# Optimization experiments

Hardware: AMD Instinct MI355X
Metric: run time of the kernel (lower is better)

Reference implementation:

```python
import jax, jax.numpy as jnp
import numpy as np

T, B, N = 1000, 64, 512
DT = 0.01
EL, VR, TR, TINF = -0.07, -0.07, -0.06, -0.05
A_VAL = 2.6239240169525146
A1_VAL = -0.015625353902578354
A2_VAL = -1.0590057373046875
B_VAL = 12.77495288848877
G_VAL = 45.24007797241211
K1, K2 = 200.0, 20.0
R1, R2 = 0.3858567178249359, -1.1421641111373901
C = 1.0


def setup_inputs() -> dict:
    key = jax.random.key(0)
    x = jax.random.normal(key, (T, B, N), dtype=jnp.float32)
    linear = jnp.ones((1, N), jnp.float32)
    a = jnp.full((1, N), A_VAL, jnp.float32)
    A1 = jnp.full((1, N), A1_VAL * C, jnp.float32)
    A2 = jnp.full((1, N), A2_VAL * C, jnp.float32)
    return {"x": x, "linear": linear, "a": a, "A1": A1, "A2": A2}


def _spike(v):
    # Heaviside step (forward of SurrGradSpike)
    return (v > 0).astype(v.dtype)


def reference(x, linear, a, A1, A2):
    G = G_VAL * C

    def step(state, xt):
        V, i1, i2, Thr = state
        i1 = i1 - K1 * i1 * DT
        i2 = i2 - K2 * i2 * DT
        V = V + DT * (linear * xt + i1 + i2 - G * (V - EL)) / C
        Thr = Thr + DT * (a * (V - EL) - B_VAL * (Thr - TINF))
        spk = _spike(V - Thr)
        i1 = (1.0 - spk) * i1 + spk * (R1 * i1 + A1)
        i2 = (1.0 - spk) * i2 + spk * (R2 * i2 + A2)
        Thr = (1.0 - spk) * Thr + spk * jnp.maximum(Thr, TR)
        V = (1.0 - spk) * V + spk * VR
        return (V, i1, i2, Thr), spk

    Bd, Nd = x.shape[1], x.shape[2]
    init = (
        jnp.full((Bd, Nd), EL, x.dtype),   # V
        jnp.zeros((Bd, Nd), x.dtype),      # i1
        jnp.zeros((Bd, Nd), x.dtype),      # i2
        jnp.full((Bd, Nd), TINF, x.dtype), # Thr
    )
    _, spikes = jax.lax.scan(step, init, x)
    return spikes  # [T, B, N] (original returns np.array of per-step spikes)
```

## Files before the change

kernel.cpp:

```cpp
#include <hip/hip_runtime.h>


#define T_STEPS 1000
#define B_DIM 64
#define N_DIM 512
#define BN (B_DIM * N_DIM)

#define K_CHUNK 20
#define NCHUNK (T_STEPS / K_CHUNK)

typedef const __attribute__((address_space(1))) void* gp_t;
typedef __attribute__((address_space(3))) void* lp_t;
typedef float f32x4 __attribute__((ext_vector_type(4)));

__device__ __forceinline__ void raw_barrier() {
    asm volatile("s_barrier" ::: "memory");
}

struct Consts {
    float k200, k20, kDT, kEL, kG, kTINF, kB, kR1, kR2, kTR;
};

__device__ __forceinline__ float mn_step(float xt, float lin, float av,
                                         float A1v, float A2v, const Consts& K,
                                         float& V, float& i1, float& i2,
                                         float& Thr)
{
#pragma clang fp contract(off)
    i1 = i1 - (K.k200 * i1) * K.kDT;
    i2 = i2 - (K.k20  * i2) * K.kDT;
    float p  = lin * xt;
    float q  = p + i1;
    float r  = q + i2;
    float e  = V - K.kEL;
    float g  = K.kG * e;
    float s  = r - g;
    float d  = K.kDT * s;
    V = V + d;
    float e2 = V - K.kEL;
    float u  = av * e2;
    float w  = Thr - K.kTINF;
    float bw = K.kB * w;
    float s2 = u - bw;
    float d2 = K.kDT * s2;
    Thr = Thr + d2;
    float diff = V - Thr;
    bool  sb   = diff > 0.0f;
    float spk  = sb ? 1.0f : 0.0f;
    float i1r = (K.kR1 * i1) + A1v;
    float i2r = (K.kR2 * i2) + A2v;
    i1  = sb ? i1r : i1;
    i2  = sb ? i2r : i2;
    float tm = fmaxf(Thr, K.kTR);
    Thr = sb ? tm : Thr;
    V   = sb ? K.kEL : V;
    return spk;
}

__global__ __launch_bounds__(128) void mn_neuron_kernel(
    const float* __restrict__ x, const float* __restrict__ linear,
    const float* __restrict__ a, const float* __restrict__ A1,
    const float* __restrict__ A2, float* __restrict__ out)
{
#pragma clang fp contract(off)
    __shared__ float xb_buf[2][K_CHUNK][64];
    __shared__ float sb_buf[2][K_CHUNK][64];

    const int lane = threadIdx.x & 63;
    const int wid  = threadIdx.x >> 6;
    const int blk  = blockIdx.x;

    if (wid == 1) {
        const float* pl = x + (size_t)(lane >> 4) * BN
                            + (size_t)blk * 64 + (size_t)(lane & 15) * 4;
        float* outp = out + (size_t)blk * 64;

        auto issue = [&](int k) {
            const float* pc = pl + (size_t)(k * K_CHUNK) * BN;
            float* dst = &xb_buf[k & 1][0][0];
#pragma unroll
            for (int s5 = 0; s5 < K_CHUNK / 4; ++s5) {
                __builtin_amdgcn_global_load_lds(
                    (gp_t)(pc + (size_t)(s5 * 4) * BN),
                    (lp_t)(dst + s5 * 4 * 64), 16, 0, 0);
            }
        };

        const int r0 = lane >> 4;
        const int c4 = (lane & 15) * 4;
        auto flush = [&](int k) {
            const int kb = k & 1;
#pragma unroll
            for (int pz = 0; pz < K_CHUNK / 4; ++pz) {
                const int row = pz * 4 + r0;
                const f32x4 v = *reinterpret_cast<const f32x4*>(
                    &sb_buf[kb][row][c4]);
                f32x4* dp = reinterpret_cast<f32x4*>(
                    outp + (size_t)(k * K_CHUNK + row) * BN + c4);
                __builtin_nontemporal_store(v, dp);
            }
        };

        issue(0);
        asm volatile("s_waitcnt vmcnt(0)" ::: "memory");
        raw_barrier();

        for (int c = 0; c < NCHUNK; ++c) {
            if (c + 1 < NCHUNK) issue(c + 1);
            if (c >= 1)         flush(c - 1);
            asm volatile("s_waitcnt vmcnt(0) lgkmcnt(0)" ::: "memory");
            raw_barrier();
        }
        flush(NCHUNK - 1);
    } else {
        const int idx = blk * 64 + lane;
        const int n   = idx & (N_DIM - 1);

        const float lin = linear[n];
        const float av  = a[n];
        const float A1v = A1[n];
        const float A2v = A2[n];

        Consts K = {200.0f, 20.0f, 0.01f, -0.07f,
                    45.24007797241211f, -0.05f, 12.77495288848877f,
                    0.3858567178249359f, -1.1421641111373901f, -0.06f};
        asm volatile("" : "+s"(K.k200), "+s"(K.k20), "+s"(K.kDT),
                          "+s"(K.kEL), "+s"(K.kG), "+s"(K.kTINF),
                          "+s"(K.kB), "+s"(K.kR1), "+s"(K.kR2), "+s"(K.kTR));

        float V   = K.kEL;
        float i1  = 0.0f;
        float i2  = 0.0f;
        float Thr = K.kTINF;

        asm volatile("s_setprio 1" ::: "memory");
        raw_barrier();

        for (int c = 0; c < NCHUNK; ++c) {
            const float* src = &xb_buf[c & 1][0][lane];
            float*       dst = &sb_buf[c & 1][0][lane];
#pragma unroll
            for (int j = 0; j < K_CHUNK; ++j) {
                float xt  = src[j * 64];
                float spk = mn_step(xt, lin, av, A1v, A2v, K, V, i1, i2, Thr);
                dst[j * 64] = spk;
            }
            asm volatile("s_waitcnt lgkmcnt(0)" ::: "memory");
            raw_barrier();
        }
    }
}

extern "C" void kernel_launch(void* const* d_in, const int* in_sizes, int n_in,
                              void* d_out, int out_size, void* d_ws, size_t ws_size,
                              hipStream_t stream) {
    const float* x      = (const float*)d_in[0];
    const float* linear = (const float*)d_in[1];
    const float* a      = (const float*)d_in[2];
    const float* A1     = (const float*)d_in[3];
    const float* A2     = (const float*)d_in[4];
    float* out = (float*)d_out;

    mn_neuron_kernel<<<BN / 64, 128, 0, stream>>>(x, linear, a, A1, A2, out);
}
```

Baseline: 232.1 us.

## Deepen x prefetch to four LDS buffers and register-pipeline LDS reads

The loader wave now keeps three chunks of x in flight across four LDS buffers, using partial vmcnt waits instead of draining all loads each chunk. The compute wave keeps a rolling four-value register window of upcoming inputs, including the head of the next chunk, so LDS read latency sits off the serial recurrence chain. The goal is to hide global-to-LDS and LDS-to-register latency behind the per-step dependency chain. In exchange, the inner loop is no longer fully unrolled (unroll 1), which adds loop overhead, and LDS use grows.

```diff
diff --git a/kernel.cpp b/kernel.cpp
--- a/kernel.cpp
+++ b/kernel.cpp
@@ -8,6 +8,7 @@
 
 #define K_CHUNK 20
 #define NCHUNK (T_STEPS / K_CHUNK)
+#define NBUF 4
 
 typedef const __attribute__((address_space(1))) void* gp_t;
 typedef __attribute__((address_space(3))) void* lp_t;
@@ -57,13 +58,13 @@
     return spk;
 }
 
-__global__ __launch_bounds__(128) void mn_neuron_kernel(
+__global__ __launch_bounds__(128, 1) void mn_neuron_kernel(
     const float* __restrict__ x, const float* __restrict__ linear,
     const float* __restrict__ a, const float* __restrict__ A1,
     const float* __restrict__ A2, float* __restrict__ out)
 {
 #pragma clang fp contract(off)
-    __shared__ float xb_buf[2][K_CHUNK][64];
+    __shared__ float xb_buf[NBUF][K_CHUNK][64];
     __shared__ float sb_buf[2][K_CHUNK][64];
 
     const int lane = threadIdx.x & 63;
@@ -77,7 +78,7 @@
 
         auto issue = [&](int k) {
             const float* pc = pl + (size_t)(k * K_CHUNK) * BN;
-            float* dst = &xb_buf[k & 1][0][0];
+            float* dst = &xb_buf[k & (NBUF - 1)][0][0];
 #pragma unroll
             for (int s5 = 0; s5 < K_CHUNK / 4; ++s5) {
                 __builtin_amdgcn_global_load_lds(
@@ -101,14 +102,19 @@
             }
         };
 
-        issue(0);
-        asm volatile("s_waitcnt vmcnt(0)" ::: "memory");
+        issue(0); issue(1); issue(2);
+        asm volatile("s_waitcnt vmcnt(5)" ::: "memory");
         raw_barrier();
 
         for (int c = 0; c < NCHUNK; ++c) {
-            if (c + 1 < NCHUNK) issue(c + 1);
-            if (c >= 1)         flush(c - 1);
-            asm volatile("s_waitcnt vmcnt(0) lgkmcnt(0)" ::: "memory");
+            if (c + 3 < NCHUNK) issue(c + 3);
+            if (c <= NCHUNK - 4) {
+                asm volatile("s_waitcnt vmcnt(5)" ::: "memory");
+            } else {
+                asm volatile("s_waitcnt vmcnt(0)" ::: "memory");
+            }
+            if (c >= 1) flush(c - 1);
+            asm volatile("s_waitcnt lgkmcnt(0)" ::: "memory");
             raw_barrier();
         }
         flush(NCHUNK - 1);
@@ -136,14 +142,38 @@
         asm volatile("s_setprio 1" ::: "memory");
         raw_barrier();
 
+        const float* c0 = &xb_buf[0][0][lane];
+        float X0 = c0[0 * 64];
+        float X1 = c0[1 * 64];
+        float X2 = c0[2 * 64];
+        float X3 = c0[3 * 64];
+
         for (int c = 0; c < NCHUNK; ++c) {
-            const float* src = &xb_buf[c & 1][0][lane];
+            const float* cur = &xb_buf[c & (NBUF - 1)][0][lane];
+            const float* nxt = &xb_buf[(c + 1) & (NBUF - 1)][0][lane];
             float*       dst = &sb_buf[c & 1][0][lane];
-#pragma unroll
-            for (int j = 0; j < K_CHUNK; ++j) {
-                float xt  = src[j * 64];
-                float spk = mn_step(xt, lin, av, A1v, A2v, K, V, i1, i2, Thr);
-                dst[j * 64] = spk;
+
+#pragma unroll 1
+            for (int i = 0; i < 8; ++i) {
+                float p0 = cur[(2 * i + 4) * 64];
+                float p1 = cur[(2 * i + 5) * 64];
+                float s0 = mn_step(X0, lin, av, A1v, A2v, K, V, i1, i2, Thr);
+                dst[(2 * i) * 64] = s0;
+                float s1 = mn_step(X1, lin, av, A1v, A2v, K, V, i1, i2, Thr);
+                dst[(2 * i + 1) * 64] = s1;
+                X0 = X2; X1 = X3; X2 = p0; X3 = p1;
+            }
+            {
+                float p0 = nxt[0 * 64];
+                float p1 = nxt[1 * 64];
+                dst[16 * 64] = mn_step(X0, lin, av, A1v, A2v, K, V, i1, i2, Thr);
+                dst[17 * 64] = mn_step(X1, lin, av, A1v, A2v, K, V, i1, i2, Thr);
+                X0 = X2; X1 = X3; X2 = p0; X3 = p1;
+                p0 = nxt[2 * 64];
+                p1 = nxt[3 * 64];
+                dst[18 * 64] = mn_step(X0, lin, av, A1v, A2v, K, V, i1, i2, Thr);
+                dst[19 * 64] = mn_step(X1, lin, av, A1v, A2v, K, V, i1, i2, Thr);
+                X0 = X2; X1 = X3; X2 = p0; X3 = p1;
             }
             asm volatile("s_waitcnt lgkmcnt(0)" ::: "memory");
             raw_barrier();
```

After: 237.1 us. 2.2% more time.

## Speculatively compute both spike and no-spike paths to shorten the serial dependency chain

Applied to the files above, without the earlier changes.

Restructures the per-neuron recurrence so the state update is computed for both outcomes of the previous step's spike (reset and no-reset). The previous spike then only selects between results, which takes the post-spike reset out of the critical latency chain. This roughly doubles the ALU work per step and raises register pressure. It also adds a launch-bounds minimum of one block per CU. It must keep bit-exact equivalence with the reference ordering of float operations.

```diff
diff --git a/kernel.cpp b/kernel.cpp
--- a/kernel.cpp
+++ b/kernel.cpp
@@ -21,43 +21,59 @@
     float k200, k20, kDT, kEL, kG, kTINF, kB, kR1, kR2, kTR;
 };
 
-__device__ __forceinline__ float mn_step(float xt, float lin, float av,
-                                         float A1v, float A2v, const Consts& K,
-                                         float& V, float& i1, float& i2,
-                                         float& Thr)
+__device__ __forceinline__ float mn_step_spec(
+    float xt, float lin, float av, float A1v, float A2v, const Consts& K,
+    float& V1, float& T1, float& tm_,
+    float& i1d, float& i1r, float& i2d, float& i2r, bool& sbp)
 {
 #pragma clang fp contract(off)
-    i1 = i1 - (K.k200 * i1) * K.kDT;
-    i2 = i2 - (K.k20  * i2) * K.kDT;
-    float p  = lin * xt;
-    float q  = p + i1;
-    float r  = q + i2;
-    float e  = V - K.kEL;
-    float g  = K.kG * e;
-    float s  = r - g;
-    float d  = K.kDT * s;
-    V = V + d;
-    float e2 = V - K.kEL;
-    float u  = av * e2;
-    float w  = Thr - K.kTINF;
-    float bw = K.kB * w;
-    float s2 = u - bw;
-    float d2 = K.kDT * s2;
-    Thr = Thr + d2;
-    float diff = V - Thr;
-    bool  sb   = diff > 0.0f;
-    float spk  = sb ? 1.0f : 0.0f;
-    float i1r = (K.kR1 * i1) + A1v;
-    float i2r = (K.kR2 * i2) + A2v;
-    i1  = sb ? i1r : i1;
-    i2  = sb ? i2r : i2;
-    float tm = fmaxf(Thr, K.kTR);
-    Thr = sb ? tm : Thr;
-    V   = sb ? K.kEL : V;
+    float a1n = i1d - (K.k200 * i1d) * K.kDT;
+    float a1s = i1r - (K.k200 * i1r) * K.kDT;
+    float a2n = i2d - (K.k20  * i2d) * K.kDT;
+    float a2s = i2r - (K.k20  * i2r) * K.kDT;
+    float p   = lin * xt;
+    float qn  = p + a1n;
+    float qs  = p + a1s;
+    float rn  = qn + a2n;
+    float rs  = qs + a2s;
+    float en  = V1 - K.kEL;
+    float gn  = K.kG * en;
+    float sn  = rn - gn;
+    float dn  = K.kDT * sn;
+    float dsp = K.kDT * rs;
+    float Vn  = V1 + dn;
+    float Vs  = K.kEL + dsp;
+    float e2n = Vn - K.kEL;
+    float e2s = Vs - K.kEL;
+    float un  = av * e2n;
+    float us  = av * e2s;
+    float wn  = T1  - K.kTINF;
+    float ws  = tm_ - K.kTINF;
+    float bn  = K.kB * wn;
+    float bs  = K.kB * ws;
+    float s2n = un - bn;
+    float s2s = us - bs;
+    float d2n = K.kDT * s2n;
+    float d2s = K.kDT * s2s;
+    float T1n = T1  + d2n;
+    float T1s = tm_ + d2s;
+    float dfn = Vn - T1n;
+    float dfs = Vs - T1s;
+    float diff = sbp ? dfs : dfn;
+    V1  = sbp ? Vs  : Vn;
+    T1  = sbp ? T1s : T1n;
+    i1d = sbp ? a1s : a1n;
+    i2d = sbp ? a2s : a2n;
+    bool  sb  = diff > 0.0f;
+    float spk = sb ? 1.0f : 0.0f;
+    sbp = sb;
+    tm_ = fmaxf(T1, K.kTR);
+    i1r = (K.kR1 * i1d) + A1v;
+    i2r = (K.kR2 * i2d) + A2v;
     return spk;
 }
 
-__global__ __launch_bounds__(128) void mn_neuron_kernel(
+__global__ __launch_bounds__(128, 1) void mn_neuron_kernel(
     const float* __restrict__ x, const float* __restrict__ linear,
     const float* __restrict__ a, const float* __restrict__ A1,
     const float* __restrict__ A2, float* __restrict__ out)
@@ -128,10 +144,14 @@
                           "+s"(K.kEL), "+s"(K.kG), "+s"(K.kTINF),
                           "+s"(K.kB), "+s"(K.kR1), "+s"(K.kR2), "+s"(K.kTR));
 
-        float V   = K.kEL;
-        float i1  = 0.0f;
-        float i2  = 0.0f;
-        float Thr = K.kTINF;
+        float V1  = K.kEL;
+        float T1  = K.kTINF;
+        float tm_ = fmaxf(K.kTINF, K.kTR);
+        float i1d = 0.0f;
+        float i1r = (K.kR1 * 0.0f) + A1v;
+        float i2d = 0.0f;
+        float i2r = (K.kR2 * 0.0f) + A2v;
+        bool  sbp = false;
 
         asm volatile("s_setprio 1" ::: "memory");
         raw_barrier();
@@ -142,7 +162,8 @@
 #pragma unroll
             for (int j = 0; j < K_CHUNK; ++j) {
                 float xt  = src[j * 64];
-                float spk = mn_step(xt, lin, av, A1v, A2v, K, V, i1, i2, Thr);
+                float spk = mn_step_spec(xt, lin, av, A1v, A2v, K,
+                                         V1, T1, tm_, i1d, i1r, i2d, i2r, sbp);
                 dst[j * 64] = spk;
             }
             asm volatile("s_waitcnt lgkmcnt(0)" ::: "memory");
```

Result: slower. 246.8 us (+6.4%).

## Process four neurons per compute lane with 256-column blocks

Applied to the files above, without the earlier changes.

Each block now covers 256 columns instead of 64, and every compute lane carries four independent neuron states through the recurrence. This gives the sequential dependency chain instruction-level parallelism and cuts the block count by four, and the loader wave now moves full 1 KB rows per time step. The trade-off is 128 blocks instead of 512 on a 256-CU device, which leaves fewer waves per CU and fewer CUs occupied, plus four times the LDS per block.

```diff
diff --git a/kernel.cpp b/kernel.cpp
--- a/kernel.cpp
+++ b/kernel.cpp
@@ -8,6 +8,7 @@
 
 #define K_CHUNK 20
 #define NCHUNK (T_STEPS / K_CHUNK)
+#define CPB 256
 
 typedef const __attribute__((address_space(1))) void* gp_t;
 typedef __attribute__((address_space(3))) void* lp_t;
@@ -57,46 +58,42 @@
     return spk;
 }
 
-__global__ __launch_bounds__(128) void mn_neuron_kernel(
+__global__ __launch_bounds__(128, 1) void mn_neuron_kernel(
     const float* __restrict__ x, const float* __restrict__ linear,
     const float* __restrict__ a, const float* __restrict__ A1,
     const float* __restrict__ A2, float* __restrict__ out)
 {
 #pragma clang fp contract(off)
-    __shared__ float xb_buf[2][K_CHUNK][64];
-    __shared__ float sb_buf[2][K_CHUNK][64];
+    __shared__ float xb_buf[2][K_CHUNK][CPB];
+    __shared__ float sb_buf[2][K_CHUNK][CPB];
 
     const int lane = threadIdx.x & 63;
     const int wid  = threadIdx.x >> 6;
     const int blk  = blockIdx.x;
 
     if (wid == 1) {
-        const float* pl = x + (size_t)(lane >> 4) * BN
-                            + (size_t)blk * 64 + (size_t)(lane & 15) * 4;
-        float* outp = out + (size_t)blk * 64;
+        const float* pl = x + (size_t)blk * CPB + (size_t)lane * 4;
+        float* outp = out + (size_t)blk * CPB;
 
         auto issue = [&](int k) {
             const float* pc = pl + (size_t)(k * K_CHUNK) * BN;
             float* dst = &xb_buf[k & 1][0][0];
 #pragma unroll
-            for (int s5 = 0; s5 < K_CHUNK / 4; ++s5) {
+            for (int r = 0; r < K_CHUNK; ++r) {
                 __builtin_amdgcn_global_load_lds(
-                    (gp_t)(pc + (size_t)(s5 * 4) * BN),
-                    (lp_t)(dst + s5 * 4 * 64), 16, 0, 0);
+                    (gp_t)(pc + (size_t)r * BN),
+                    (lp_t)(dst + r * CPB), 16, 0, 0);
             }
         };
 
-        const int r0 = lane >> 4;
-        const int c4 = (lane & 15) * 4;
         auto flush = [&](int k) {
             const int kb = k & 1;
 #pragma unroll
-            for (int pz = 0; pz < K_CHUNK / 4; ++pz) {
-                const int row = pz * 4 + r0;
+            for (int r = 0; r < K_CHUNK; ++r) {
                 const f32x4 v = *reinterpret_cast<const f32x4*>(
-                    &sb_buf[kb][row][c4]);
+                    &sb_buf[kb][r][lane * 4]);
                 f32x4* dp = reinterpret_cast<f32x4*>(
-                    outp + (size_t)(k * K_CHUNK + row) * BN + c4);
+                    outp + (size_t)(k * K_CHUNK + r) * BN + (size_t)lane * 4);
                 __builtin_nontemporal_store(v, dp);
             }
         };
@@ -113,13 +110,10 @@
         }
         flush(NCHUNK - 1);
     } else {
-        const int idx = blk * 64 + lane;
-        const int n   = idx & (N_DIM - 1);
+        const int i0 = blk * CPB + lane;
 
-        const float lin = linear[n];
-        const float av  = a[n];
-        const float A1v = A1[n];
-        const float A2v = A2[n];
+        float lin[4], av[4], A1r[4], A2r[4];
+        float V[4], i1[4], i2[4], Thr[4];
 
         Consts K = {200.0f, 20.0f, 0.01f, -0.07f,
                     45.24007797241211f, -0.05f, 12.77495288848877f,
@@ -128,10 +122,18 @@
                           "+s"(K.kEL), "+s"(K.kG), "+s"(K.kTINF),
                           "+s"(K.kB), "+s"(K.kR1), "+s"(K.kR2), "+s"(K.kTR));
 
-        float V   = K.kEL;
-        float i1  = 0.0f;
-        float i2  = 0.0f;
-        float Thr = K.kTINF;
+#pragma unroll
+        for (int k = 0; k < 4; ++k) {
+            const int n = (i0 + 64 * k) & (N_DIM - 1);
+            lin[k] = linear[n];
+            av[k]  = a[n];
+            A1r[k] = A1[n];
+            A2r[k] = A2[n];
+            V[k]   = K.kEL;
+            i1[k]  = 0.0f;
+            i2[k]  = 0.0f;
+            Thr[k] = K.kTINF;
+        }
 
         asm volatile("s_setprio 1" ::: "memory");
         raw_barrier();
@@ -139,11 +141,15 @@
         for (int c = 0; c < NCHUNK; ++c) {
             const float* src = &xb_buf[c & 1][0][lane];
             float*       dst = &sb_buf[c & 1][0][lane];
+#pragma unroll 2
+            for (int j = 0; j < K_CHUNK; ++j) {
 #pragma unroll
-            for (int j = 0; j < K_CHUNK; ++j) {
-                float xt  = src[j * 64];
-                float spk = mn_step(xt, lin, av, A1v, A2v, K, V, i1, i2, Thr);
-                dst[j * 64] = spk;
+                for (int k = 0; k < 4; ++k) {
+                    float xt  = src[j * CPB + 64 * k];
+                    float spk = mn_step(xt, lin[k], av[k], A1r[k], A2r[k], K,
+                                        V[k], i1[k], i2[k], Thr[k]);
+                    dst[j * CPB + 64 * k] = spk;
+                }
             }
             asm volatile("s_waitcnt lgkmcnt(0)" ::: "memory");
             raw_barrier();
@@ -161,5 +167,5 @@
     const float* A2     = (const float*)d_in[4];
     float* out = (float*)d_out;
 
-    mn_neuron_kernel<<<BN / 64, 128, 0, stream>>>(x, linear, a, A1, A2, out);
+    mn_neuron_kernel<<<BN / CPB, 128, 0, stream>>>(x, linear, a, A1, A2, out);
 }
```

After: 375.3 us. 1.62x slower.
